# Optimization experiments

Hardware: AMD Instinct MI355X
Metric: run time of the kernel (lower is better)

Reference implementation:

```python
import jax, jax.numpy as jnp
import numpy as np

B, D, C_IN, C_OUT = 256, 8, 2, 4


def setup_inputs() -> dict:
    key = jax.random.key(0)
    k1, k2, k3, k4 = jax.random.split(key, 4)
    rho = jax.random.normal(k1, (B, C_IN * D * D, C_IN * D * D), dtype=jnp.float32)
    ux = jax.random.normal(k2, (D, D), dtype=jnp.float32)
    uy = jax.random.normal(k3, (D, D), dtype=jnp.float32)
    uc = jax.random.normal(k4, (C_OUT, C_OUT), dtype=jnp.float32)
    return {"rho": rho, "ux": ux, "uy": uy, "uc": uc}


def _insert_channels(rho, d, c_in, c_out):
    # Faithful port of _InsertChannels: move each (channel f, pixel i,j) row/col
    # index to channel f + (c_out - c_in) in the enlarged register.
    b = rho.shape[0]
    x = jnp.arange(c_in * d * d)
    f = x // (d * d)                       # channel index
    i = (x % (d * d)) // d                 # row pixel
    j = x % d                              # col pixel
    new_idx = i * d + j + (f + (c_out - c_in)) * d * d  # [c_in*d^2]
    big = jnp.zeros((b, c_out * d * d, c_out * d * d), dtype=rho.dtype)
    # Indices are a bijection onto a sub-block, so add == set (matches
    # index_put_(..., accumulate=True) in torch).
    return big.at[:, new_idx[:, None], new_idx[None, :]].add(rho)


def reference(rho, ux, uy, uc):
    d = ux.shape[0]
    c_out = uc.shape[0]
    c_in = rho.shape[1] // (d * d)
    # channel insertion (c_in < c_out path)
    rho_big = _insert_channels(rho, d, c_in, c_out)        # [b, C, C], C = c_out*d^2
    # u = kron(uc, kron(ux, uy))
    u = jnp.kron(uc, jnp.kron(ux, uy))                     # [C, C]
    # new_rho = u @ rho @ u^H (real float32 -> conj is identity, transpose only)
    u_rho = jnp.einsum('pq,bqr->bpr', u, rho_big)
    new_rho = jnp.einsum('bpr,sr->bps', u_rho, u)
    return new_rho
```

## Files before the change

kernel.cpp:

```cpp
#include <hip/hip_runtime.h>


#define TPB 512

__global__ __launch_bounds__(TPB, 2) void qconv_fused(
    const float* __restrict__ rho,
    const float* __restrict__ ux,
    const float* __restrict__ uy,
    const float* __restrict__ uc,
    float* __restrict__ out)
{
    __shared__ alignas(16) float L[4][64][68];

    const int tid = threadIdx.x;
    const int b   = blockIdx.x;

    if (tid < 256) {
        const int w    = tid >> 6;
        const int lane = tid & 63;
        const int c1   = w >> 1, c2 = w & 1;
        const int px   = lane >> 3, qx = lane & 7;

        const float* rb = rho + (size_t)b * 16384
                        + (size_t)((c1 << 6) + (px << 3)) * 128 + (c2 << 6) + (qx << 3);

        float X[64], Y[64];

#pragma unroll
        for (int py = 0; py < 8; ++py) {
            float4 lo = *(const float4*)(rb + py * 128);
            float4 hi = *(const float4*)(rb + py * 128 + 4);
            X[py*8+0]=lo.x; X[py*8+1]=lo.y; X[py*8+2]=lo.z; X[py*8+3]=lo.w;
            X[py*8+4]=hi.x; X[py*8+5]=hi.y; X[py*8+6]=hi.z; X[py*8+7]=hi.w;
        }

#pragma unroll
        for (int py = 0; py < 8; ++py)
#pragma unroll
            for (int j = 0; j < 8; ++j) {
                float acc = 0.f;
#pragma unroll
                for (int k = 0; k < 8; ++k) acc += uy[j*8+k] * X[py*8+k];
                Y[py*8+j] = acc;
            }
#pragma unroll
        for (int i = 0; i < 8; ++i)
#pragma unroll
            for (int j = 0; j < 8; ++j) {
                float acc = 0.f;
#pragma unroll
                for (int k = 0; k < 8; ++k) acc += uy[i*8+k] * Y[k*8+j];
                X[i*8+j] = acc;
            }

#pragma unroll
        for (int e = 0; e < 64; ++e) L[w][e][lane] = X[e];
        __asm__ volatile("s_waitcnt lgkmcnt(0)" ::: "memory");
#pragma unroll
        for (int f4 = 0; f4 < 16; ++f4) {
            float4 v = *(const float4*)&L[w][lane][f4 * 4];
            X[f4*4+0]=v.x; X[f4*4+1]=v.y; X[f4*4+2]=v.z; X[f4*4+3]=v.w;
        }

#pragma unroll
        for (int p = 0; p < 8; ++p)
#pragma unroll
            for (int j = 0; j < 8; ++j) {
                float acc = 0.f;
#pragma unroll
                for (int k = 0; k < 8; ++k) acc += ux[j*8+k] * X[p*8+k];
                Y[p*8+j] = acc;
            }
#pragma unroll
        for (int i = 0; i < 8; ++i)
#pragma unroll
            for (int j = 0; j < 8; ++j) {
                float acc = 0.f;
#pragma unroll
                for (int k = 0; k < 8; ++k) acc += ux[i*8+k] * Y[k*8+j];
                X[i*8+j] = acc;
            }

        {
            const int pyp = lane >> 3, qyp = lane & 7;
#pragma unroll
            for (int px_ = 0; px_ < 8; ++px_)
#pragma unroll
                for (int qx_ = 0; qx_ < 8; ++qx_)
                    L[w][px_*8+pyp][qx_*8+qyp] = X[px_*8+qx_];
        }
    }

    __syncthreads();

    float e0[4], e1[4];
#pragma unroll
    for (int c = 0; c < 4; ++c) { e0[c] = uc[c*4+2]; e1[c] = uc[c*4+3]; }

    float* ob = out + (size_t)b * 65536;
#pragma unroll
    for (int i = 0; i < 2; ++i) {
        const int g  = tid + TPB * i;
        const int sp = g >> 4;
        const int qg = g & 15;
        float4 wv[4];
#pragma unroll
        for (int ww = 0; ww < 4; ++ww) wv[ww] = *(const float4*)&L[ww][sp][qg * 4];
#pragma unroll
        for (int c = 0; c < 4; ++c) {
#pragma unroll
            for (int cs = 0; cs < 4; ++cs) {
                const float k00 = e0[c]*e0[cs], k01 = e0[c]*e1[cs];
                const float k10 = e1[c]*e0[cs], k11 = e1[c]*e1[cs];
                float4 v;
                v.x = k00*wv[0].x + k01*wv[1].x + k10*wv[2].x + k11*wv[3].x;
                v.y = k00*wv[0].y + k01*wv[1].y + k10*wv[2].y + k11*wv[3].y;
                v.z = k00*wv[0].z + k01*wv[1].z + k10*wv[2].z + k11*wv[3].z;
                v.w = k00*wv[0].w + k01*wv[1].w + k10*wv[2].w + k11*wv[3].w;
                *(float4*)&ob[(size_t)((c*64 + sp) * 256 + cs*64 + qg*4)] = v;
            }
        }
    }
}

extern "C" void kernel_launch(void* const* d_in, const int* in_sizes, int n_in,
                              void* d_out, int out_size, void* d_ws, size_t ws_size,
                              hipStream_t stream) {
    const float* rho = (const float*)d_in[0];
    const float* ux  = (const float*)d_in[1];
    const float* uy  = (const float*)d_in[2];
    const float* uc  = (const float*)d_in[3];
    float* out = (float*)d_out;
    qconv_fused<<<dim3(256), dim3(TPB), 0, stream>>>(rho, ux, uy, uc, out);
}
```

Baseline: 90.14 us.

## Interleave final ux stage with output writes in four synchronized slabs

```diff
diff --git a/kernel.cpp b/kernel.cpp
--- a/kernel.cpp
+++ b/kernel.cpp
@@ -12,20 +12,30 @@
 {
     __shared__ alignas(16) float L[4][64][68];
 
-    const int tid = threadIdx.x;
-    const int b   = blockIdx.x;
+    const int tid  = threadIdx.x;
+    const int b    = blockIdx.x;
+    const int w    = tid >> 6;
+    const int lane = tid & 63;
+    const int pyp  = lane >> 3, qyp = lane & 7;
 
-    if (tid < 256) {
-        const int w    = tid >> 6;
-        const int lane = tid & 63;
-        const int c1   = w >> 1, c2 = w & 1;
-        const int px   = lane >> 3, qx = lane & 7;
+    const int qg  = tid & 15;
+    const int csh = (tid >> 4) & 1;
+    const int spl = tid >> 5;
 
+    float e0[4], e1[4];
+#pragma unroll
+    for (int c = 0; c < 4; ++c) { e0[c] = uc[c*4+2]; e1[c] = uc[c*4+3]; }
+    float* ob = out + (size_t)b * 65536;
+
+    float Y[64];
+
+    if (w < 4) {
+        const int c1 = w >> 1, c2 = w & 1;
+        const int px = lane >> 3, qx = lane & 7;
         const float* rb = rho + (size_t)b * 16384
                         + (size_t)((c1 << 6) + (px << 3)) * 128 + (c2 << 6) + (qx << 3);
 
-        float X[64], Y[64];
-
+        float X[64];
 #pragma unroll
         for (int py = 0; py < 8; ++py) {
             float4 lo = *(const float4*)(rb + py * 128);
@@ -33,7 +43,6 @@
             X[py*8+0]=lo.x; X[py*8+1]=lo.y; X[py*8+2]=lo.z; X[py*8+3]=lo.w;
             X[py*8+4]=hi.x; X[py*8+5]=hi.y; X[py*8+6]=hi.z; X[py*8+7]=hi.w;
         }
-
 #pragma unroll
         for (int py = 0; py < 8; ++py)
 #pragma unroll
@@ -52,7 +61,6 @@
                 for (int k = 0; k < 8; ++k) acc += uy[i*8+k] * Y[k*8+j];
                 X[i*8+j] = acc;
             }
-
 #pragma unroll
         for (int e = 0; e < 64; ++e) L[w][e][lane] = X[e];
         __asm__ volatile("s_waitcnt lgkmcnt(0)" ::: "memory");
@@ -61,7 +69,6 @@
             float4 v = *(const float4*)&L[w][lane][f4 * 4];
             X[f4*4+0]=v.x; X[f4*4+1]=v.y; X[f4*4+2]=v.z; X[f4*4+3]=v.w;
         }
-
 #pragma unroll
         for (int p = 0; p < 8; ++p)
 #pragma unroll
@@ -71,45 +78,34 @@
                 for (int k = 0; k < 8; ++k) acc += ux[j*8+k] * X[p*8+k];
                 Y[p*8+j] = acc;
             }
-#pragma unroll
-        for (int i = 0; i < 8; ++i)
-#pragma unroll
-            for (int j = 0; j < 8; ++j) {
-                float acc = 0.f;
-#pragma unroll
-                for (int k = 0; k < 8; ++k) acc += ux[i*8+k] * Y[k*8+j];
-                X[i*8+j] = acc;
-            }
-
-        {
-            const int pyp = lane >> 3, qyp = lane & 7;
-#pragma unroll
-            for (int px_ = 0; px_ < 8; ++px_)
-#pragma unroll
-                for (int qx_ = 0; qx_ < 8; ++qx_)
-                    L[w][px_*8+pyp][qx_*8+qyp] = X[px_*8+qx_];
-        }
     }
 
-    __syncthreads();
+#pragma unroll
+    for (int s = 0; s < 4; ++s) {
+        if (w < 4) {
+#pragma unroll
+            for (int i2 = 0; i2 < 2; ++i2) {
+                const int i = 2*s + i2;
+#pragma unroll
+                for (int j = 0; j < 8; ++j) {
+                    float acc = 0.f;
+#pragma unroll
+                    for (int k = 0; k < 8; ++k) acc += ux[i*8+k] * Y[k*8+j];
+                    L[w][i*8+pyp][j*8+qyp] = acc;
+                }
+            }
+        }
+        __syncthreads();
 
-    float e0[4], e1[4];
-#pragma unroll
-    for (int c = 0; c < 4; ++c) { e0[c] = uc[c*4+2]; e1[c] = uc[c*4+3]; }
-
-    float* ob = out + (size_t)b * 65536;
-#pragma unroll
-    for (int i = 0; i < 2; ++i) {
-        const int g  = tid + TPB * i;
-        const int sp = g >> 4;
-        const int qg = g & 15;
+        const int sp = 16*s + spl;
         float4 wv[4];
 #pragma unroll
         for (int ww = 0; ww < 4; ++ww) wv[ww] = *(const float4*)&L[ww][sp][qg * 4];
 #pragma unroll
         for (int c = 0; c < 4; ++c) {
 #pragma unroll
-            for (int cs = 0; cs < 4; ++cs) {
+            for (int cs2 = 0; cs2 < 2; ++cs2) {
+                const int cs = 2*csh + cs2;
                 const float k00 = e0[c]*e0[cs], k01 = e0[c]*e1[cs];
                 const float k10 = e1[c]*e0[cs], k11 = e1[c]*e1[cs];
                 float4 v;
```

Measured after the change: 88.90 us. Within noise of the previous version (-1.4%).
